# Kernel optimization log

Measured on AMD Instinct MI355X. Metric: run time of the kernel, lower is better.

Reference implementation:

```python
import jax, jax.numpy as jnp
import numpy as np

B, S, E = 4, 1024, 1024
H, DH = 16, 64
P = 64  # prompt length
MASKED_BIAS = -10000.0


def setup_inputs() -> dict:
    key = jax.random.key(0)
    ks = jax.random.split(key, 9)
    return {
        "hidden_states": jax.random.normal(ks[0], (B, S, E), jnp.float32),
        "promptKey": jax.random.normal(ks[1], (B, H, P, DH), jnp.float32),
        "promptValue": jax.random.normal(ks[2], (B, H, P, DH), jnp.float32),
        "textualKey": jax.random.normal(ks[3], (B, H, S, DH), jnp.float32),
        "textualValue": jax.random.normal(ks[4], (B, H, S, DH), jnp.float32),
        "promptMask": jnp.ones((B, 1, S, P), jnp.bool_),
        "c_attn_w": jax.random.normal(ks[5], (E, 3 * E), jnp.float32) * 0.02,
        "c_attn_b": jnp.zeros((3 * E,), jnp.float32),
        "c_proj_w": jax.random.normal(ks[6], (E, E), jnp.float32) * 0.02,
        "c_proj_b": jnp.zeros((E,), jnp.float32),
    }


def _split_heads(t):
    # [B, S, E] -> [B, H, S, DH]
    b, s, _ = t.shape
    return t.reshape(b, s, H, DH).transpose(0, 2, 1, 3)


def reference(hidden_states, promptKey, promptValue, textualKey, textualValue,
              promptMask, c_attn_w, c_attn_b, c_proj_w, c_proj_b):
    qkv = hidden_states @ c_attn_w + c_attn_b          # [B,S,3E]
    q, k, v = jnp.split(qkv, 3, axis=-1)
    q, k, v = _split_heads(q), _split_heads(k), _split_heads(v)  # [B,H,S,DH]

    # scores against prompt KV, textual KV, and elementwise self term
    promptW = jnp.einsum("bhsd,bhpd->bhsp", q, promptKey)       # [B,H,S,P]
    textW = jnp.einsum("bhsd,bhtd->bhst", q, textualKey)        # [B,H,S,S]
    selfW = jnp.sum(q * k, axis=-1, keepdims=True)              # [B,H,S,1]
    attn_weights = jnp.concatenate((promptW, textW, selfW), axis=-1)
    attn_weights = attn_weights / jnp.sqrt(jnp.float32(DH))

    # non-residual causal mask: bias[qlen-qlen:qlen, 1:klen+1] -> strictly lower tri
    causal = jnp.tri(S, S, -1, dtype=bool)                      # [S,S]
    self_mask = jnp.ones((S, 1), dtype=bool)
    causal_self = jnp.concatenate((causal, self_mask), axis=-1)[None, None]  # [1,1,S,S+1]
    full_mask = jnp.concatenate(
        (promptMask, jnp.broadcast_to(causal_self, (B, 1, S, S + 1))), axis=-1)
    attn_weights = jnp.where(full_mask, attn_weights, MASKED_BIAS)
    attn_weights = jax.nn.softmax(attn_weights, axis=-1)

    wSelf = attn_weights[..., -1:]                              # [B,H,S,1]
    wRest = attn_weights[..., :-1]                              # [B,H,S,P+S]
    valuePast = jnp.concatenate((promptValue, textualValue), axis=-2)  # [B,H,P+S,DH]
    attn_output = jnp.einsum("bhsk,bhkd->bhsd", wRest, valuePast) + wSelf * v

    # merge heads and output projection
    attn_output = attn_output.transpose(0, 2, 1, 3).reshape(B, S, E)
    return attn_output @ c_proj_w + c_proj_b
```

## Files before the change

### kernel.cpp

```cpp
#include <hip/hip_runtime.h>
#include <hip/hip_bf16.h>
#include <stdint.h>

#define H_ 16
#define DH_ 64
#define S_ 1024
#define B_ 4
#define E_ 1024
#define P_ 64
#define BH_ (B_ * H_)
#define KV_ (P_ + S_)
#define NT_ 17
#define TILE_ELEMS 4096

typedef __attribute__((ext_vector_type(8))) short short8;
typedef __attribute__((ext_vector_type(4))) float floatx4;

#define MFMA_BF16(a, b, c) __builtin_amdgcn_mfma_f32_16x16x32_bf16((a), (b), (c), 0, 0, 0)

__device__ __forceinline__ float bf2f(unsigned short u) {
    union { float f; uint32_t i; } x;
    x.i = ((uint32_t)u) << 16;
    return x.f;
}
__device__ __forceinline__ unsigned short f2bf(float f) {
    uint32_t i = __float_as_uint(f);
    uint32_t r = (i + 0x7fffu + ((i >> 16) & 1u)) >> 16;
    return (unsigned short)r;
}

__device__ __forceinline__ void gl_lds16(const void* g, void* l) {
    __builtin_amdgcn_global_load_lds(
        (const __attribute__((address_space(1))) uint32_t*)g,
        (__attribute__((address_space(3))) uint32_t*)l, 16, 0, 0);
}

__global__ void cast_f2b(const float* __restrict__ in,
                         unsigned short* __restrict__ out, int n4) {
    int i = blockIdx.x * 256 + threadIdx.x;
    if (i >= n4) return;
    float4 v = ((const float4*)in)[i];
    ushort4 o;
    o.x = f2bf(v.x); o.y = f2bf(v.y); o.z = f2bf(v.z); o.w = f2bf(v.w);
    ((ushort4*)out)[i] = o;
}

__global__ void transpose_f2b(const float* __restrict__ in,
                              unsigned short* __restrict__ out, int R, int C) {
    __shared__ float t[32][33];
    int tx = threadIdx.x, ty = threadIdx.y;
    int c0 = blockIdx.x * 32, r0 = blockIdx.y * 32;
#pragma unroll
    for (int i = 0; i < 4; ++i)
        t[ty + i * 8][tx] = in[(size_t)(r0 + ty + i * 8) * C + c0 + tx];
    __syncthreads();
#pragma unroll
    for (int i = 0; i < 4; ++i)
        out[(size_t)(c0 + ty + i * 8) * R + r0 + tx] = f2bf(t[tx][ty + i * 8]);
}

__global__ void pack_kv(const float* __restrict__ pK, const float* __restrict__ tK,
                        const float* __restrict__ pV, const float* __restrict__ tV,
                        unsigned short* __restrict__ Kp, unsigned short* __restrict__ Vp) {
    int gid0 = blockIdx.x * 256 + threadIdx.x;
    int half = gid0 / (BH_ * 8704);
    int gid = gid0 % (BH_ * 8704);
    int bh = gid / 8704, rem = gid % 8704;
    int t = rem / 512, r2 = rem % 512;
    int f = r2 >> 6, lane = r2 & 63;
    int nt = f >> 1, h = f & 1, quad = lane >> 4, cl = lane & 15;
    unsigned short o[8];
    if (half == 0) {
        int key = t * 64 + nt * 16 + cl;
        int dh = h * 32 + quad * 8;
        const float* src = (key < P_)
            ? pK + ((size_t)bh * P_ + key) * DH_ + dh
            : tK + ((size_t)bh * S_ + (key - P_)) * DH_ + dh;
#pragma unroll
        for (int u = 0; u < 8; ++u) o[u] = f2bf(src[u]);
        *(int4*)&Kp[(size_t)gid * 8] = *(int4*)o;
    } else {
        int dhn = nt * 16 + cl;
        int kbase = t * 64 + h * 32 + quad * 8;
        const float* src = (kbase < P_)
            ? pV + ((size_t)bh * P_ + kbase) * DH_ + dhn
            : tV + ((size_t)bh * S_ + (kbase - P_)) * DH_ + dhn;
#pragma unroll
        for (int u = 0; u < 8; ++u) o[u] = f2bf(src[(size_t)u * DH_]);
        *(int4*)&Vp[(size_t)gid * 8] = *(int4*)o;
    }
}

template <int MODE>
__global__ __launch_bounds__(256) void gemm_bt(
    const unsigned short* __restrict__ A, const unsigned short* __restrict__ Bt,
    const float* __restrict__ bias, float* __restrict__ Cout,
    unsigned short* __restrict__ Qo, unsigned short* __restrict__ Ko,
    unsigned short* __restrict__ Vo, int M, int N, int K) {
    __shared__ __align__(16) unsigned short lA[128 * 64];
    __shared__ __align__(16) unsigned short lB[128 * 64];
    int tid = threadIdx.x;
    int wave = tid >> 6, lane = tid & 63, quad = lane >> 4, cl = lane & 15;
    int m0 = blockIdx.y * 128, n0 = blockIdx.x * 128;
    int wm = (wave >> 1) * 64, wn = (wave & 1) * 64;
    int srow = tid >> 2, sc8 = (tid & 3) * 8;
    floatx4 acc[4][4];
#pragma unroll
    for (int mi = 0; mi < 4; ++mi)
#pragma unroll
        for (int ni = 0; ni < 4; ++ni) acc[mi][ni] = (floatx4){0.f, 0.f, 0.f, 0.f};

    for (int k0 = 0; k0 < K; k0 += 64) {
        __syncthreads();
        {
            const unsigned short* gA = A + (size_t)(m0 + srow) * K + k0 + sc8;
            const unsigned short* gB = Bt + (size_t)(n0 + srow) * K + k0 + sc8;
#pragma unroll
            for (int hh = 0; hh < 2; ++hh) {
#pragma unroll
                for (int pt = 0; pt < 2; ++pt) {
                    size_t go = (size_t)pt * 64 * K + hh * 32;
                    int lo = hh * 8192 + pt * 4096 + tid * 16;
                    gl_lds16(gA + go, (char*)lA + lo);
                    gl_lds16(gB + go, (char*)lB + lo);
                }
            }
        }
        __syncthreads();
#pragma unroll
        for (int kk = 0; kk < 2; ++kk) {
            short8 af[4], bfr[4];
#pragma unroll
            for (int mi = 0; mi < 4; ++mi)
                af[mi] = *(const short8*)&lA[kk * 4096 + (wm + mi * 16 + cl) * 32 + quad * 8];
#pragma unroll
            for (int ni = 0; ni < 4; ++ni)
                bfr[ni] = *(const short8*)&lB[kk * 4096 + (wn + ni * 16 + cl) * 32 + quad * 8];
#pragma unroll
            for (int mi = 0; mi < 4; ++mi)
#pragma unroll
                for (int ni = 0; ni < 4; ++ni)
                    acc[mi][ni] = MFMA_BF16(af[mi], bfr[ni], acc[mi][ni]);
        }
    }

#pragma unroll
    for (int ni = 0; ni < 4; ++ni) {
        int ncol = n0 + wn + ni * 16 + cl;
        float bv = bias[ncol];
#pragma unroll
        for (int mi = 0; mi < 4; ++mi) {
#pragma unroll
            for (int r = 0; r < 4; ++r) {
                int mrow = m0 + wm + mi * 16 + quad * 4 + r;
                float v = acc[mi][ni][r] + bv;
                if (MODE == 0) {
                    Cout[(size_t)mrow * N + ncol] = v;
                } else {
                    int which = ncol >> 10, e = ncol & 1023;
                    int hh = e >> 6, dh = e & 63;
                    int b = mrow >> 10, s = mrow & 1023;
                    size_t idx = ((size_t)(b * H_ + hh) * S_ + s) * DH_ + dh;
                    unsigned short* dst = (which == 0) ? Qo : ((which == 1) ? Ko : Vo);
                    dst[idx] = f2bf(v);
                }
            }
        }
    }
}

__global__ __launch_bounds__(256) void attn_k(
    const unsigned short* __restrict__ Q, const unsigned short* __restrict__ Kc,
    const unsigned short* __restrict__ Vc, const unsigned short* __restrict__ Kp,
    const unsigned short* __restrict__ Vp, unsigned short* __restrict__ Aout) {
    __shared__ __align__(16) unsigned short lK[TILE_ELEMS];
    __shared__ __align__(16) unsigned short lV[TILE_ELEMS];
    __shared__ __align__(16) unsigned short lP[4][16 * 72];
    int tid = threadIdx.x, wave = tid >> 6, lane = tid & 63;
    int quad = lane >> 4, cl = lane & 15;
    int bx = blockIdx.x, bh = blockIdx.y;
    int qb = bx * 64 + wave * 16;
    int b = bh >> 4, h = bh & 15;
    const unsigned short* Qb = Q + (size_t)bh * S_ * DH_;
    const unsigned short* Kb = Kc + (size_t)bh * S_ * DH_;
    const unsigned short* Vb = Vc + (size_t)bh * S_ * DH_;
    const unsigned short* Kpb = Kp + (size_t)bh * NT_ * TILE_ELEMS;
    const unsigned short* Vpb = Vp + (size_t)bh * NT_ * TILE_ELEMS;
    unsigned short* lp = lP[wave];

    short8 a0 = *(const short8*)(Qb + (size_t)(qb + cl) * DH_ + quad * 8);
    short8 a1 = *(const short8*)(Qb + (size_t)(qb + cl) * DH_ + quad * 8 + 32);

    float lsum[4] = {0.f, 0.f, 0.f, 0.f};
    floatx4 O[4];
#pragma unroll
    for (int nt = 0; nt < 4; ++nt) O[nt] = (floatx4){0.f, 0.f, 0.f, 0.f};

    int T = bx + 2;
    int so = wave * 1024 + lane * 16;
    for (int t = 0; t < T; ++t) {
        __syncthreads();
        {
            const char* gK = (const char*)(Kpb + (size_t)t * TILE_ELEMS);
            const char* gV = (const char*)(Vpb + (size_t)t * TILE_ELEMS);
            gl_lds16(gK + so, (char*)lK + so);
            gl_lds16(gK + 4096 + so, (char*)lK + 4096 + so);
            gl_lds16(gV + so, (char*)lV + so);
            gl_lds16(gV + 4096 + so, (char*)lV + 4096 + so);
        }
        __syncthreads();

        floatx4 s[4];
#pragma unroll
        for (int nt = 0; nt < 4; ++nt) {
            s[nt] = (floatx4){0.f, 0.f, 0.f, 0.f};
            short8 k0 = *(const short8*)&lK[(nt * 2 + 0) * 512 + lane * 8];
            short8 k1 = *(const short8*)&lK[(nt * 2 + 1) * 512 + lane * 8];
            s[nt] = MFMA_BF16(a0, k0, s[nt]);
            s[nt] = MFMA_BF16(a1, k1, s[nt]);
        }
        bool diag = (t == T - 1);
        int rl = wave * 16 + quad * 4;
#pragma unroll
        for (int nt = 0; nt < 4; ++nt) {
            int col = nt * 16 + cl;
#pragma unroll
            for (int r = 0; r < 4; ++r) {
                float v = s[nt][r] * 0.125f;
                if (diag && col >= rl + r) v = -10000.0f;
                float p = __expf(v);
                lsum[r] += p;
                lp[(quad * 4 + r) * 72 + col] = f2bf(p);
            }
        }
        asm volatile("s_waitcnt lgkmcnt(0)" ::: "memory");
        short8 p0 = *(const short8*)&lp[cl * 72 + quad * 8];
        short8 p1 = *(const short8*)&lp[cl * 72 + quad * 8 + 32];
#pragma unroll
        for (int nt = 0; nt < 4; ++nt) {
            short8 v0 = *(const short8*)&lV[(nt * 2 + 0) * 512 + lane * 8];
            short8 v1 = *(const short8*)&lV[(nt * 2 + 1) * 512 + lane * 8];
            O[nt] = MFMA_BF16(p0, v0, O[nt]);
            O[nt] = MFMA_BF16(p1, v1, O[nt]);
        }
    }

#pragma unroll
    for (int r = 0; r < 4; ++r) {
        float rs = lsum[r];
        rs += __shfl_xor(rs, 1, 16);
        rs += __shfl_xor(rs, 2, 16);
        rs += __shfl_xor(rs, 4, 16);
        rs += __shfl_xor(rs, 8, 16);
        int row = qb + quad * 4 + r;
        const unsigned short* qp = Qb + (size_t)row * DH_ + cl * 4;
        const unsigned short* kp = Kb + (size_t)row * DH_ + cl * 4;
        float d = 0.f;
#pragma unroll
        for (int u = 0; u < 4; ++u) d += bf2f(qp[u]) * bf2f(kp[u]);
        d += __shfl_xor(d, 1, 16);
        d += __shfl_xor(d, 2, 16);
        d += __shfl_xor(d, 4, 16);
        d += __shfl_xor(d, 8, 16);
        float ps = __expf(d * 0.125f);
        float linv = 1.0f / (rs + ps);
#pragma unroll
        for (int nt = 0; nt < 4; ++nt) {
            float vv = bf2f(Vb[(size_t)row * DH_ + nt * 16 + cl]);
            float o = (O[nt][r] + ps * vv) * linv;
            Aout[((size_t)b * S_ + row) * E_ + h * DH_ + nt * 16 + cl] = f2bf(o);
        }
    }
}

extern "C" void kernel_launch(void* const* d_in, const int* in_sizes, int n_in,
                              void* d_out, int out_size, void* d_ws, size_t ws_size,
                              hipStream_t stream) {
    const float* hidden = (const float*)d_in[0];
    const float* pK = (const float*)d_in[1];
    const float* pV = (const float*)d_in[2];
    const float* tK = (const float*)d_in[3];
    const float* tV = (const float*)d_in[4];
    const float* cw = (const float*)d_in[6];
    const float* cb = (const float*)d_in[7];
    const float* pw = (const float*)d_in[8];
    const float* pb = (const float*)d_in[9];
    float* out = (float*)d_out;

    unsigned short* ws = (unsigned short*)d_ws;
    unsigned short* Wt1 = ws;
    unsigned short* Wt2 = Wt1 + (size_t)3072 * 1024;
    unsigned short* Ah  = Wt2 + (size_t)1024 * 1024;
    unsigned short* Qw  = Ah + (size_t)4096 * 1024;
    unsigned short* Kw  = Qw + (size_t)BH_ * S_ * DH_;
    unsigned short* Vw  = Kw + (size_t)BH_ * S_ * DH_;
    unsigned short* Kp  = Vw + (size_t)BH_ * S_ * DH_;
    unsigned short* Vp  = Kp + (size_t)BH_ * NT_ * TILE_ELEMS;
    unsigned short* At  = Ah;

    dim3 tb(32, 8);
    cast_f2b<<<4096, 256, 0, stream>>>(hidden, Ah, 4096 * 1024 / 4);
    transpose_f2b<<<dim3(3072 / 32, 1024 / 32), tb, 0, stream>>>(cw, Wt1, 1024, 3072);
    transpose_f2b<<<dim3(1024 / 32, 1024 / 32), tb, 0, stream>>>(pw, Wt2, 1024, 1024);
    pack_kv<<<4352, 256, 0, stream>>>(pK, tK, pV, tV, Kp, Vp);
    gemm_bt<1><<<dim3(3072 / 128, 4096 / 128), 256, 0, stream>>>(
        Ah, Wt1, cb, nullptr, Qw, Kw, Vw, 4096, 3072, 1024);
    attn_k<<<dim3(S_ / 64, BH_), 256, 0, stream>>>(Qw, Kw, Vw, Kp, Vp, At);
    gemm_bt<0><<<dim3(1024 / 128, 4096 / 128), 256, 0, stream>>>(
        At, Wt2, pb, out, nullptr, nullptr, nullptr, 4096, 1024, 1024);
}
```

Measured before the change: 231.0 us.

## Fuse prep kernels, double-buffer GEMM loads, balance causal attention, retile projection

Merges the cast, two transposes and KV packing into one prep launch to cut launch overhead. The GEMM now double-buffers its global-to-LDS loads, waiting on vmcnt so the next tile's load overlaps the current tile's MFMAs. It is templated on tile size so the output projection uses 128x64 tiles, giving more blocks. The attention kernel pairs query block p with block 15-p in one workgroup to even out causal work per block, which halves the grid to 8x64 and risks lower occupancy.

```diff
diff --git a/kernel.cpp b/kernel.cpp
--- a/kernel.cpp
+++ b/kernel.cpp
@@ -35,113 +35,137 @@
         (__attribute__((address_space(3))) uint32_t*)l, 16, 0, 0);
 }
 
-__global__ void cast_f2b(const float* __restrict__ in,
-                         unsigned short* __restrict__ out, int n4) {
-    int i = blockIdx.x * 256 + threadIdx.x;
-    if (i >= n4) return;
-    float4 v = ((const float4*)in)[i];
-    ushort4 o;
-    o.x = f2bf(v.x); o.y = f2bf(v.y); o.z = f2bf(v.z); o.w = f2bf(v.w);
-    ((ushort4*)out)[i] = o;
-}
-
-__global__ void transpose_f2b(const float* __restrict__ in,
-                              unsigned short* __restrict__ out, int R, int C) {
+#define BARRIER() asm volatile("s_barrier" ::: "memory")
+#define WAIT_VM(n) asm volatile("s_waitcnt vmcnt(" #n ")" ::: "memory")
+
+__global__ void prep(const float* __restrict__ hidden, const float* __restrict__ cw,
+                     const float* __restrict__ pw, const float* __restrict__ pK,
+                     const float* __restrict__ tK, const float* __restrict__ pV,
+                     const float* __restrict__ tV, unsigned short* __restrict__ Ah,
+                     unsigned short* __restrict__ Wt1, unsigned short* __restrict__ Wt2,
+                     unsigned short* __restrict__ Kp, unsigned short* __restrict__ Vp) {
     __shared__ float t[32][33];
-    int tx = threadIdx.x, ty = threadIdx.y;
-    int c0 = blockIdx.x * 32, r0 = blockIdx.y * 32;
-#pragma unroll
-    for (int i = 0; i < 4; ++i)
-        t[ty + i * 8][tx] = in[(size_t)(r0 + ty + i * 8) * C + c0 + tx];
-    __syncthreads();
-#pragma unroll
-    for (int i = 0; i < 4; ++i)
-        out[(size_t)(c0 + ty + i * 8) * R + r0 + tx] = f2bf(t[tx][ty + i * 8]);
-}
-
-__global__ void pack_kv(const float* __restrict__ pK, const float* __restrict__ tK,
-                        const float* __restrict__ pV, const float* __restrict__ tV,
-                        unsigned short* __restrict__ Kp, unsigned short* __restrict__ Vp) {
-    int gid0 = blockIdx.x * 256 + threadIdx.x;
-    int half = gid0 / (BH_ * 8704);
-    int gid = gid0 % (BH_ * 8704);
-    int bh = gid / 8704, rem = gid % 8704;
-    int t = rem / 512, r2 = rem % 512;
-    int f = r2 >> 6, lane = r2 & 63;
-    int nt = f >> 1, h = f & 1, quad = lane >> 4, cl = lane & 15;
-    unsigned short o[8];
-    if (half == 0) {
-        int key = t * 64 + nt * 16 + cl;
-        int dh = h * 32 + quad * 8;
-        const float* src = (key < P_)
-            ? pK + ((size_t)bh * P_ + key) * DH_ + dh
-            : tK + ((size_t)bh * S_ + (key - P_)) * DH_ + dh;
-#pragma unroll
-        for (int u = 0; u < 8; ++u) o[u] = f2bf(src[u]);
-        *(int4*)&Kp[(size_t)gid * 8] = *(int4*)o;
+    int bid = blockIdx.x, tid = threadIdx.x;
+    if (bid < 4096) {
+        int i = bid * 256 + tid;
+        float4 v = ((const float4*)hidden)[i];
+        ushort4 o;
+        o.x = f2bf(v.x); o.y = f2bf(v.y); o.z = f2bf(v.z); o.w = f2bf(v.w);
+        ((ushort4*)Ah)[i] = o;
+    } else if (bid < 8192) {
+        const float* in; unsigned short* out; int R, C, bxx, byy;
+        if (bid < 7168) { int i = bid - 4096; in = cw; out = Wt1; R = 1024; C = 3072; bxx = i % 96; byy = i / 96; }
+        else            { int i = bid - 7168; in = pw; out = Wt2; R = 1024; C = 1024; bxx = i % 32; byy = i / 32; }
+        int tx = tid & 31, ty = tid >> 5;
+        int c0 = bxx * 32, r0 = byy * 32;
+#pragma unroll
+        for (int i = 0; i < 4; ++i)
+            t[ty + i * 8][tx] = in[(size_t)(r0 + ty + i * 8) * C + c0 + tx];
+        __syncthreads();
+#pragma unroll
+        for (int i = 0; i < 4; ++i)
+            out[(size_t)(c0 + ty + i * 8) * R + r0 + tx] = f2bf(t[tx][ty + i * 8]);
     } else {
-        int dhn = nt * 16 + cl;
-        int kbase = t * 64 + h * 32 + quad * 8;
-        const float* src = (kbase < P_)
-            ? pV + ((size_t)bh * P_ + kbase) * DH_ + dhn
-            : tV + ((size_t)bh * S_ + (kbase - P_)) * DH_ + dhn;
-#pragma unroll
-        for (int u = 0; u < 8; ++u) o[u] = f2bf(src[(size_t)u * DH_]);
-        *(int4*)&Vp[(size_t)gid * 8] = *(int4*)o;
+        int gid0 = (bid - 8192) * 256 + tid;
+        int half = gid0 / (BH_ * 8704);
+        int gid = gid0 % (BH_ * 8704);
+        int bh = gid / 8704, rem = gid % 8704;
+        int tt = rem / 512, r2 = rem % 512;
+        int f = r2 >> 6, lane = r2 & 63;
+        int nt = f >> 1, h = f & 1, quad = lane >> 4, cl = lane & 15;
+        unsigned short o[8];
+        if (half == 0) {
+            int key = tt * 64 + nt * 16 + cl;
+            int dh = h * 32 + quad * 8;
+            const float* src = (key < P_)
+                ? pK + ((size_t)bh * P_ + key) * DH_ + dh
+                : tK + ((size_t)bh * S_ + (key - P_)) * DH_ + dh;
+#pragma unroll
+            for (int u = 0; u < 8; ++u) o[u] = f2bf(src[u]);
+            *(int4*)&Kp[(size_t)gid * 8] = *(int4*)o;
+        } else {
+            int dhn = nt * 16 + cl;
+            int kbase = tt * 64 + h * 32 + quad * 8;
+            const float* src = (kbase < P_)
+                ? pV + ((size_t)bh * P_ + kbase) * DH_ + dhn
+                : tV + ((size_t)bh * S_ + (kbase - P_)) * DH_ + dhn;
+#pragma unroll
+            for (int u = 0; u < 8; ++u) o[u] = f2bf(src[(size_t)u * DH_]);
+            *(int4*)&Vp[(size_t)gid * 8] = *(int4*)o;
+        }
     }
 }
 
-template <int MODE>
+template <int MODE, int TM, int TN>
 __global__ __launch_bounds__(256) void gemm_bt(
     const unsigned short* __restrict__ A, const unsigned short* __restrict__ Bt,
     const float* __restrict__ bias, float* __restrict__ Cout,
     unsigned short* __restrict__ Qo, unsigned short* __restrict__ Ko,
     unsigned short* __restrict__ Vo, int M, int N, int K) {
-    __shared__ __align__(16) unsigned short lA[128 * 64];
-    __shared__ __align__(16) unsigned short lB[128 * 64];
+    constexpr int RPA = TM / 64, RPB = TN / 64;
+    constexpr int NLOADS = (RPA + RPB) * 2;
+    constexpr int MI = (TN == 128) ? 4 : 2;
+    __shared__ __align__(16) unsigned short lA[2][TM * 64];
+    __shared__ __align__(16) unsigned short lB[2][TN * 64];
     int tid = threadIdx.x;
     int wave = tid >> 6, lane = tid & 63, quad = lane >> 4, cl = lane & 15;
-    int m0 = blockIdx.y * 128, n0 = blockIdx.x * 128;
-    int wm = (wave >> 1) * 64, wn = (wave & 1) * 64;
+    int m0 = blockIdx.y * TM, n0 = blockIdx.x * TN;
+    int wm = (TN == 128) ? (wave >> 1) * 64 : wave * 32;
+    int wn = (TN == 128) ? (wave & 1) * 64 : 0;
     int srow = tid >> 2, sc8 = (tid & 3) * 8;
-    floatx4 acc[4][4];
-#pragma unroll
-    for (int mi = 0; mi < 4; ++mi)
+    floatx4 acc[MI][4];
+#pragma unroll
+    for (int mi = 0; mi < MI; ++mi)
 #pragma unroll
         for (int ni = 0; ni < 4; ++ni) acc[mi][ni] = (floatx4){0.f, 0.f, 0.f, 0.f};
 
-    for (int k0 = 0; k0 < K; k0 += 64) {
-        __syncthreads();
-        {
-            const unsigned short* gA = A + (size_t)(m0 + srow) * K + k0 + sc8;
-            const unsigned short* gB = Bt + (size_t)(n0 + srow) * K + k0 + sc8;
-#pragma unroll
-            for (int hh = 0; hh < 2; ++hh) {
-#pragma unroll
-                for (int pt = 0; pt < 2; ++pt) {
-                    size_t go = (size_t)pt * 64 * K + hh * 32;
-                    int lo = hh * 8192 + pt * 4096 + tid * 16;
-                    gl_lds16(gA + go, (char*)lA + lo);
-                    gl_lds16(gB + go, (char*)lB + lo);
-                }
-            }
-        }
-        __syncthreads();
+    const unsigned short* gA0 = A + (size_t)(m0 + srow) * K + sc8;
+    const unsigned short* gB0 = Bt + (size_t)(n0 + srow) * K + sc8;
+
+    auto issue = [&](int k0, int buf) {
+#pragma unroll
+        for (int hh = 0; hh < 2; ++hh) {
+#pragma unroll
+            for (int pt = 0; pt < RPA; ++pt)
+                gl_lds16(gA0 + (size_t)k0 + (size_t)pt * 64 * K + hh * 32,
+                         (char*)lA[buf] + hh * TM * 64 + pt * 4096 + tid * 16);
+#pragma unroll
+            for (int pt = 0; pt < RPB; ++pt)
+                gl_lds16(gB0 + (size_t)k0 + (size_t)pt * 64 * K + hh * 32,
+                         (char*)lB[buf] + hh * TN * 64 + pt * 4096 + tid * 16);
+        }
+    };
+    auto compute = [&](int buf) {
 #pragma unroll
         for (int kk = 0; kk < 2; ++kk) {
-            short8 af[4], bfr[4];
-#pragma unroll
-            for (int mi = 0; mi < 4; ++mi)
-                af[mi] = *(const short8*)&lA[kk * 4096 + (wm + mi * 16 + cl) * 32 + quad * 8];
+            short8 af[MI], bfr[4];
+#pragma unroll
+            for (int mi = 0; mi < MI; ++mi)
+                af[mi] = *(const short8*)&lA[buf][kk * TM * 32 + (wm + mi * 16 + cl) * 32 + quad * 8];
 #pragma unroll
             for (int ni = 0; ni < 4; ++ni)
-                bfr[ni] = *(const short8*)&lB[kk * 4096 + (wn + ni * 16 + cl) * 32 + quad * 8];
-#pragma unroll
-            for (int mi = 0; mi < 4; ++mi)
+                bfr[ni] = *(const short8*)&lB[buf][kk * TN * 32 + (wn + ni * 16 + cl) * 32 + quad * 8];
+#pragma unroll
+            for (int mi = 0; mi < MI; ++mi)
 #pragma unroll
                 for (int ni = 0; ni < 4; ++ni)
                     acc[mi][ni] = MFMA_BF16(af[mi], bfr[ni], acc[mi][ni]);
         }
+    };
+
+    int nT = K >> 6;
+    issue(0, 0);
+    for (int t = 0; t < nT; ++t) {
+        int buf = t & 1;
+        if (t + 1 < nT) {
+            issue((t + 1) << 6, buf ^ 1);
+            if constexpr (NLOADS == 8) WAIT_VM(8); else WAIT_VM(6);
+        } else {
+            WAIT_VM(0);
+        }
+        BARRIER();
+        compute(buf);
+        BARRIER();
     }
 
 #pragma unroll
@@ -149,7 +173,7 @@
         int ncol = n0 + wn + ni * 16 + cl;
         float bv = bias[ncol];
 #pragma unroll
-        for (int mi = 0; mi < 4; ++mi) {
+        for (int mi = 0; mi < MI; ++mi) {
 #pragma unroll
             for (int r = 0; r < 4; ++r) {
                 int mrow = m0 + wm + mi * 16 + quad * 4 + r;
@@ -178,8 +202,7 @@
     __shared__ __align__(16) unsigned short lP[4][16 * 72];
     int tid = threadIdx.x, wave = tid >> 6, lane = tid & 63;
     int quad = lane >> 4, cl = lane & 15;
-    int bx = blockIdx.x, bh = blockIdx.y;
-    int qb = bx * 64 + wave * 16;
+    int p = blockIdx.x, bh = blockIdx.y;
     int b = bh >> 4, h = bh & 15;
     const unsigned short* Qb = Q + (size_t)bh * S_ * DH_;
     const unsigned short* Kb = Kc + (size_t)bh * S_ * DH_;
@@ -187,88 +210,93 @@
     const unsigned short* Kpb = Kp + (size_t)bh * NT_ * TILE_ELEMS;
     const unsigned short* Vpb = Vp + (size_t)bh * NT_ * TILE_ELEMS;
     unsigned short* lp = lP[wave];
-
-    short8 a0 = *(const short8*)(Qb + (size_t)(qb + cl) * DH_ + quad * 8);
-    short8 a1 = *(const short8*)(Qb + (size_t)(qb + cl) * DH_ + quad * 8 + 32);
-
-    float lsum[4] = {0.f, 0.f, 0.f, 0.f};
-    floatx4 O[4];
-#pragma unroll
-    for (int nt = 0; nt < 4; ++nt) O[nt] = (floatx4){0.f, 0.f, 0.f, 0.f};
-
-    int T = bx + 2;
     int so = wave * 1024 + lane * 16;
-    for (int t = 0; t < T; ++t) {
-        __syncthreads();
-        {
-            const char* gK = (const char*)(Kpb + (size_t)t * TILE_ELEMS);
-            const char* gV = (const char*)(Vpb + (size_t)t * TILE_ELEMS);
-            gl_lds16(gK + so, (char*)lK + so);
-            gl_lds16(gK + 4096 + so, (char*)lK + 4096 + so);
-            gl_lds16(gV + so, (char*)lV + so);
-            gl_lds16(gV + 4096 + so, (char*)lV + 4096 + so);
-        }
-        __syncthreads();
-
-        floatx4 s[4];
-#pragma unroll
-        for (int nt = 0; nt < 4; ++nt) {
-            s[nt] = (floatx4){0.f, 0.f, 0.f, 0.f};
-            short8 k0 = *(const short8*)&lK[(nt * 2 + 0) * 512 + lane * 8];
-            short8 k1 = *(const short8*)&lK[(nt * 2 + 1) * 512 + lane * 8];
-            s[nt] = MFMA_BF16(a0, k0, s[nt]);
-            s[nt] = MFMA_BF16(a1, k1, s[nt]);
-        }
-        bool diag = (t == T - 1);
-        int rl = wave * 16 + quad * 4;
-#pragma unroll
-        for (int nt = 0; nt < 4; ++nt) {
-            int col = nt * 16 + cl;
-#pragma unroll
-            for (int r = 0; r < 4; ++r) {
-                float v = s[nt][r] * 0.125f;
-                if (diag && col >= rl + r) v = -10000.0f;
-                float p = __expf(v);
-                lsum[r] += p;
-                lp[(quad * 4 + r) * 72 + col] = f2bf(p);
-            }
-        }
-        asm volatile("s_waitcnt lgkmcnt(0)" ::: "memory");
-        short8 p0 = *(const short8*)&lp[cl * 72 + quad * 8];
-        short8 p1 = *(const short8*)&lp[cl * 72 + quad * 8 + 32];
-#pragma unroll
-        for (int nt = 0; nt < 4; ++nt) {
-            short8 v0 = *(const short8*)&lV[(nt * 2 + 0) * 512 + lane * 8];
-            short8 v1 = *(const short8*)&lV[(nt * 2 + 1) * 512 + lane * 8];
-            O[nt] = MFMA_BF16(p0, v0, O[nt]);
-            O[nt] = MFMA_BF16(p1, v1, O[nt]);
-        }
-    }
-
-#pragma unroll
-    for (int r = 0; r < 4; ++r) {
-        float rs = lsum[r];
-        rs += __shfl_xor(rs, 1, 16);
-        rs += __shfl_xor(rs, 2, 16);
-        rs += __shfl_xor(rs, 4, 16);
-        rs += __shfl_xor(rs, 8, 16);
-        int row = qb + quad * 4 + r;
-        const unsigned short* qp = Qb + (size_t)row * DH_ + cl * 4;
-        const unsigned short* kp = Kb + (size_t)row * DH_ + cl * 4;
-        float d = 0.f;
-#pragma unroll
-        for (int u = 0; u < 4; ++u) d += bf2f(qp[u]) * bf2f(kp[u]);
-        d += __shfl_xor(d, 1, 16);
-        d += __shfl_xor(d, 2, 16);
-        d += __shfl_xor(d, 4, 16);
-        d += __shfl_xor(d, 8, 16);
-        float ps = __expf(d * 0.125f);
-        float linv = 1.0f / (rs + ps);
-#pragma unroll
-        for (int nt = 0; nt < 4; ++nt) {
-            float vv = bf2f(Vb[(size_t)row * DH_ + nt * 16 + cl]);
-            float o = (O[nt][r] + ps * vv) * linv;
-            Aout[((size_t)b * S_ + row) * E_ + h * DH_ + nt * 16 + cl] = f2bf(o);
+
+    for (int seg = 0; seg < 2; ++seg) {
+        int x = seg ? (15 - p) : p;
+        int qb = x * 64 + wave * 16;
+
+        short8 a0 = *(const short8*)(Qb + (size_t)(qb + cl) * DH_ + quad * 8);
+        short8 a1 = *(const short8*)(Qb + (size_t)(qb + cl) * DH_ + quad * 8 + 32);
+
+        float lsum[4] = {0.f, 0.f, 0.f, 0.f};
+        floatx4 O[4];
+#pragma unroll
+        for (int nt = 0; nt < 4; ++nt) O[nt] = (floatx4){0.f, 0.f, 0.f, 0.f};
+
+        int T = x + 2;
+        for (int t = 0; t < T; ++t) {
+            __syncthreads();
+            {
+                const char* gK = (const char*)(Kpb + (size_t)t * TILE_ELEMS);
+                const char* gV = (const char*)(Vpb + (size_t)t * TILE_ELEMS);
+                gl_lds16(gK + so, (char*)lK + so);
+                gl_lds16(gK + 4096 + so, (char*)lK + 4096 + so);
+                gl_lds16(gV + so, (char*)lV + so);
+                gl_lds16(gV + 4096 + so, (char*)lV + 4096 + so);
+            }
+            __syncthreads();
+
+            floatx4 s[4];
+#pragma unroll
+            for (int nt = 0; nt < 4; ++nt) {
+                s[nt] = (floatx4){0.f, 0.f, 0.f, 0.f};
+                short8 k0 = *(const short8*)&lK[(nt * 2 + 0) * 512 + lane * 8];
+                short8 k1 = *(const short8*)&lK[(nt * 2 + 1) * 512 + lane * 8];
+                s[nt] = MFMA_BF16(a0, k0, s[nt]);
+                s[nt] = MFMA_BF16(a1, k1, s[nt]);
+            }
+            bool diag = (t == T - 1);
+            int rl = wave * 16 + quad * 4;
+#pragma unroll
+            for (int nt = 0; nt < 4; ++nt) {
+                int col = nt * 16 + cl;
+#pragma unroll
+                for (int r = 0; r < 4; ++r) {
+                    float v = s[nt][r] * 0.125f;
+                    if (diag && col >= rl + r) v = -10000.0f;
+                    float pb = __expf(v);
+                    lsum[r] += pb;
+                    lp[(quad * 4 + r) * 72 + col] = f2bf(pb);
+                }
+            }
+            asm volatile("s_waitcnt lgkmcnt(0)" ::: "memory");
+            short8 p0 = *(const short8*)&lp[cl * 72 + quad * 8];
+            short8 p1 = *(const short8*)&lp[cl * 72 + quad * 8 + 32];
+#pragma unroll
+            for (int nt = 0; nt < 4; ++nt) {
+                short8 v0 = *(const short8*)&lV[(nt * 2 + 0) * 512 + lane * 8];
+                short8 v1 = *(const short8*)&lV[(nt * 2 + 1) * 512 + lane * 8];
+                O[nt] = MFMA_BF16(p0, v0, O[nt]);
+                O[nt] = MFMA_BF16(p1, v1, O[nt]);
+            }
+        }
+
+#pragma unroll
+        for (int r = 0; r < 4; ++r) {
+            float rs = lsum[r];
+            rs += __shfl_xor(rs, 1, 16);
+            rs += __shfl_xor(rs, 2, 16);
+            rs += __shfl_xor(rs, 4, 16);
+            rs += __shfl_xor(rs, 8, 16);
+            int row = qb + quad * 4 + r;
+            const unsigned short* qp = Qb + (size_t)row * DH_ + cl * 4;
+            const unsigned short* kp = Kb + (size_t)row * DH_ + cl * 4;
+            float d = 0.f;
+#pragma unroll
+            for (int u = 0; u < 4; ++u) d += bf2f(qp[u]) * bf2f(kp[u]);
+            d += __shfl_xor(d, 1, 16);
+            d += __shfl_xor(d, 2, 16);
+            d += __shfl_xor(d, 4, 16);
+            d += __shfl_xor(d, 8, 16);
+            float ps = __expf(d * 0.125f);
+            float linv = 1.0f / (rs + ps);
+#pragma unroll
+            for (int nt = 0; nt < 4; ++nt) {
+                float vv = bf2f(Vb[(size_t)row * DH_ + nt * 16 + cl]);
+                float o = (O[nt][r] + ps * vv) * linv;
+                Aout[((size_t)b * S_ + row) * E_ + h * DH_ + nt * 16 + cl] = f2bf(o);
+            }
         }
     }
 }
@@ -298,14 +326,11 @@
     unsigned short* Vp  = Kp + (size_t)BH_ * NT_ * TILE_ELEMS;
     unsigned short* At  = Ah;
 
-    dim3 tb(32, 8);
-    cast_f2b<<<4096, 256, 0, stream>>>(hidden, Ah, 4096 * 1024 / 4);
-    transpose_f2b<<<dim3(3072 / 32, 1024 / 32), tb, 0, stream>>>(cw, Wt1, 1024, 3072);
-    transpose_f2b<<<dim3(1024 / 32, 1024 / 32), tb, 0, stream>>>(pw, Wt2, 1024, 1024);
-    pack_kv<<<4352, 256, 0, stream>>>(pK, tK, pV, tV, Kp, Vp);
-    gemm_bt<1><<<dim3(3072 / 128, 4096 / 128), 256, 0, stream>>>(
+    prep<<<12544, 256, 0, stream>>>(hidden, cw, pw, pK, tK, pV, tV,
+                                    Ah, Wt1, Wt2, Kp, Vp);
+    gemm_bt<1, 128, 128><<<dim3(3072 / 128, 4096 / 128), 256, 0, stream>>>(
         Ah, Wt1, cb, nullptr, Qw, Kw, Vw, 4096, 3072, 1024);
-    attn_k<<<dim3(S_ / 64, BH_), 256, 0, stream>>>(Qw, Kw, Vw, Kp, Vp, At);
-    gemm_bt<0><<<dim3(1024 / 128, 4096 / 128), 256, 0, stream>>>(
+    attn_k<<<dim3(8, BH_), 256, 0, stream>>>(Qw, Kw, Vw, Kp, Vp, At);
+    gemm_bt<0, 128, 64><<<dim3(1024 / 64, 4096 / 128), 256, 0, stream>>>(
         At, Wt2, pb, out, nullptr, nullptr, nullptr, 4096, 1024, 1024);
 }
```

After: 219.0 us. 1.05x faster.
